# Optimization experiments

Measured on AMD Instinct MI355X. Metric: run time of the kernel, lower is better.

The kernel has to match this reference:

```python
import jax, jax.numpy as jnp
import numpy as np

B, L_DEC, V = 8, 256, 32000
L_SRC = 512
V_EXT = 32128


def setup_inputs() -> dict:
    key = jax.random.key(0)
    k1, k2, k3, k4 = jax.random.split(key, 4)
    dist_t = jax.random.uniform(k1, (B, L_DEC, V), dtype=jnp.float32)
    p_gen = jax.random.uniform(k2, (B, L_DEC, 1), dtype=jnp.float32)
    alph_t = jax.random.uniform(k3, (B, L_SRC, L_DEC), dtype=jnp.float32)
    batch_vocab = jnp.zeros((V_EXT,), dtype=jnp.float32)  # only shape[0] is used
    pointer = jax.random.randint(k4, (B, L_SRC), 0, V_EXT, dtype=jnp.int32)
    return {"dist_t": dist_t, "p_gen": p_gen, "alph_t": alph_t,
            "batch_vocab": batch_vocab, "pointer": pointer}


def reference(dist_t, p_gen, alph_t, batch_vocab, pointer):
    v_ext = batch_vocab.shape[0]
    nb, nl, ndim = dist_t.shape
    # p_gen * [vocab ; zeros padding up to extended vocab]
    prob_vocab = p_gen * jnp.pad(dist_t, ((0, 0), (0, 0), (0, v_ext - ndim)))
    # torch builds a dense one-hot [B, L_src, V_ext] and does bmm(alpha^T, one_hot).
    # Mathematically: copyp[b, t, v] = sum_{s : pointer[b,s]==v} alpha[b, s, t]
    # -> scatter-add of attention weights into pointed vocab slots.
    alpha_td = jnp.swapaxes(alph_t, 1, 2)  # [B, L_dec, L_src]

    def scatter_one(a_td, ptr):  # a_td: [L_dec, L_src], ptr: [L_src]
        return jnp.zeros((a_td.shape[0], v_ext), a_td.dtype).at[:, ptr].add(a_td)

    copyp = jax.vmap(scatter_one)(alpha_td, pointer)  # [B, L_dec, V_ext]
    proba = prob_vocab + (1.0 - p_gen) * copyp
    return proba
```

## Files before the change

kernel.cpp:

```cpp
#include <hip/hip_runtime.h>

#define B_     8
#define L_DEC_ 256
#define V_     32000
#define L_SRC_ 512
#define V_EXT_ 32128

#define V4_    (V_ / 4)
#define VE4_   (V_EXT_ / 4)

#define HALF_  16064
#define HALF4_ (HALF_ / 4)

__global__ __launch_bounds__(512) void copynet_fused(
    const float* __restrict__ dist,
    const float* __restrict__ p_gen,
    const float* __restrict__ alph,
    const int*   __restrict__ pointer,
    float* __restrict__ out)
{
    __shared__ float cp[HALF_];

    const int row = blockIdx.x;
    const int b   = row >> 8;
    const int t   = row & (L_DEC_ - 1);
    const int tid = threadIdx.x;

    const float pg   = p_gen[row];
    const float coef = 1.0f - pg;

    const int   sIdx = b * L_SRC_ + tid;
    const int   v    = pointer[sIdx];
    const float val  = coef * alph[(size_t)sIdx * L_DEC_ + t];

    const float4* dist4 = (const float4*)(dist + (size_t)row * V_);
    float4*       out4  = (float4*)(out + (size_t)row * V_EXT_);
    float4*       cp4   = (float4*)cp;

#pragma unroll
    for (int h = 0; h < 2; ++h) {
        for (int i = tid; i < HALF4_; i += 512)
            cp4[i] = make_float4(0.f, 0.f, 0.f, 0.f);
        __syncthreads();

        const int lo = h * HALF_;
        if ((unsigned)(v - lo) < (unsigned)HALF_)
            atomicAdd(&cp[v - lo], val);
        __syncthreads();

        const int base4 = h * HALF4_;
        for (int i = tid; i < HALF4_; i += 512) {
            const int g4 = base4 + i;
            float4 r = cp4[i];
            if (g4 < V4_) {
                const float4 d = dist4[g4];
                r.x = fmaf(pg, d.x, r.x);
                r.y = fmaf(pg, d.y, r.y);
                r.z = fmaf(pg, d.z, r.z);
                r.w = fmaf(pg, d.w, r.w);
            }
            out4[g4] = r;
        }
        __syncthreads();
    }
}

extern "C" void kernel_launch(void* const* d_in, const int* in_sizes, int n_in,
                              void* d_out, int out_size, void* d_ws, size_t ws_size,
                              hipStream_t stream)
{
    const float* dist    = (const float*)d_in[0];
    const float* p_gen   = (const float*)d_in[1];
    const float* alph    = (const float*)d_in[2];
    const int*   pointer = (const int*)d_in[4];
    float* out = (float*)d_out;

    copynet_fused<<<B_ * L_DEC_, 512, 0, stream>>>(dist, p_gen, alph, pointer, out);
}
```

Before: 439.1 us.

## Replace shared-memory scatter staging with direct global atomics after streaming write

```diff
diff --git a/kernel.cpp b/kernel.cpp
--- a/kernel.cpp
+++ b/kernel.cpp
@@ -8,19 +8,17 @@
 
 #define V4_    (V_ / 4)
 #define VE4_   (V_EXT_ / 4)
+#define PAD4_  (VE4_ - V4_)
 
-#define HALF_  16064
-#define HALF4_ (HALF_ / 4)
+typedef float f32x4 __attribute__((ext_vector_type(4)));
 
-__global__ __launch_bounds__(512) void copynet_fused(
+__global__ __launch_bounds__(512, 8) void copynet_fused(
     const float* __restrict__ dist,
     const float* __restrict__ p_gen,
     const float* __restrict__ alph,
     const int*   __restrict__ pointer,
     float* __restrict__ out)
 {
-    __shared__ float cp[HALF_];
-
     const int row = blockIdx.x;
     const int b   = row >> 8;
     const int t   = row & (L_DEC_ - 1);
@@ -33,36 +31,22 @@
     const int   v    = pointer[sIdx];
     const float val  = coef * alph[(size_t)sIdx * L_DEC_ + t];
 
-    const float4* dist4 = (const float4*)(dist + (size_t)row * V_);
-    float4*       out4  = (float4*)(out + (size_t)row * V_EXT_);
-    float4*       cp4   = (float4*)cp;
+    const f32x4* dist4 = (const f32x4*)(dist + (size_t)row * V_);
+    f32x4*       out4  = (f32x4*)(out + (size_t)row * V_EXT_);
 
-#pragma unroll
-    for (int h = 0; h < 2; ++h) {
-        for (int i = tid; i < HALF4_; i += 512)
-            cp4[i] = make_float4(0.f, 0.f, 0.f, 0.f);
-        __syncthreads();
+    for (int i = tid; i < V4_; i += 512) {
+        f32x4 d = __builtin_nontemporal_load(dist4 + i);
+        d *= pg;
+        out4[i] = d;
+    }
+    if (tid < PAD4_) {
+        f32x4 z = {0.f, 0.f, 0.f, 0.f};
+        out4[V4_ + tid] = z;
+    }
 
-        const int lo = h * HALF_;
-        if ((unsigned)(v - lo) < (unsigned)HALF_)
-            atomicAdd(&cp[v - lo], val);
-        __syncthreads();
+    __syncthreads();
 
-        const int base4 = h * HALF4_;
-        for (int i = tid; i < HALF4_; i += 512) {
-            const int g4 = base4 + i;
-            float4 r = cp4[i];
-            if (g4 < V4_) {
-                const float4 d = dist4[g4];
-                r.x = fmaf(pg, d.x, r.x);
-                r.y = fmaf(pg, d.y, r.y);
-                r.z = fmaf(pg, d.z, r.z);
-                r.w = fmaf(pg, d.w, r.w);
-            }
-            out4[g4] = r;
-        }
-        __syncthreads();
-    }
+    atomicAdd(out + (size_t)row * V_EXT_ + v, val);
 }
 
 extern "C" void kernel_launch(void* const* d_in, const int* in_sizes, int n_in,
```

Measured after the change: 476.7 us. 1.09x slower.
